# Performance work log

Hardware: AMD Instinct MI355X
Metric: run time of the kernel (lower is better)

Reference implementation:

```python
import jax, jax.numpy as jnp
import numpy as np

G = 8            # n_group
C = 256          # input_dim / channels
N_MEM = C // G   # 32
ALPHA = 0.4      # w_alpha
EPS = 1e-5
SLOPE = 0.01     # LeakyReLU negative slope


def _lrelu(x):
    return jnp.where(x >= 0, x, SLOPE * x)


def _mlp(x, ws, bs):
    # torch nn.Linear convention: y = x @ W.T + b; lrelu on all but last layer
    n = len(ws)
    for i in range(n):
        x = x @ ws[i].T + bs[i]
        if i < n - 1:
            x = _lrelu(x)
    return x


def _wct(c_A, s_B, mask, ct_ws, ct_bs, mu_ws, mu_bs):
    B, Cc, H, W = c_A.shape
    n_mem = Cc // G
    # style -> per-group coloring matrices  (Get.coloring, vectorized over groups)
    s_CT = _mlp(s_B.reshape(B * G, n_mem), ct_ws, ct_bs).reshape(B, G, n_mem, n_mem)
    D = jnp.sqrt(jnp.sum(s_CT ** 2, axis=2, keepdims=True))        # [B,G,1,n_mem]
    U = s_CT / D                                                    # column-normalized
    UDU = jnp.einsum('bgij,bgkj->bgik', s_CT, U)                    # [B,G,n_mem,n_mem]
    # torch.cat(U_arr, dim=0) is group-major: index g*B+b
    eigen_s = jnp.transpose(U, (1, 0, 2, 3)).reshape(G * B, n_mem, n_mem)
    X = jnp.tile(UDU.reshape(B, Cc, n_mem), (1, 1, G)) * mask       # [B,C,C]
    s_mu = _mlp(s_B, mu_ws, mu_bs)[:, :, None, None]                # [B,C,1,1]
    # per-group covariance of mean-centered content
    c_g = jnp.transpose(c_A, (1, 0, 2, 3)).reshape(G, n_mem, B * H * W)
    c_g = c_g - jnp.mean(c_g, axis=2, keepdims=True)
    cov_c = jnp.einsum('gin,gjn->gij', c_g, c_g) / (B * H * W - 1) \
        + EPS * jnp.eye(n_mem, dtype=c_A.dtype)
    # centered content, reinterpreted as [B, C, H*W] (matches torch view/permute)
    whitend = jnp.transpose(c_g.reshape(Cc, B, H * W), (1, 0, 2))
    colored = jnp.einsum('bcd,bdn->bcn', X, whitend).reshape(B, Cc, H, W)
    out = ALPHA * (colored + s_mu) + (1.0 - ALPHA) * c_A
    return out, cov_c, eigen_s


def setup_inputs():
    key = jax.random.key(0)
    ks = jax.random.split(key, 16)
    B, H, W = 4, 128, 128
    c_A = jax.random.normal(ks[0], (B, C, H, W), dtype=jnp.float32)
    s_B = jax.random.normal(ks[1], (B, C), dtype=jnp.float32)
    # block-diagonal group mask [1, C, C]
    m = np.zeros((C, C), dtype=np.float32)
    for g in range(G):
        m[g * N_MEM:(g + 1) * N_MEM, g * N_MEM:(g + 1) * N_MEM] = 1.0
    mask = jnp.asarray(m)[None]

    def lin(k, o, i):
        return jax.random.normal(k, (o, i), dtype=jnp.float32) * (1.0 / np.sqrt(i))

    inp = {'c_A': c_A, 's_B': s_B, 'mask': mask}
    dims_ct = [(256, 32), (256, 256), (256, 256), (256, 256), (1024, 256)]
    for j, (o, i) in enumerate(dims_ct):
        inp['ct_w%d' % j] = lin(ks[2 + j], o, i)
        inp['ct_b%d' % j] = jnp.zeros((o,), dtype=jnp.float32)
    dims_mu = [(256, 256), (256, 256), (256, 256)]
    for j, (o, i) in enumerate(dims_mu):
        inp['mu_w%d' % j] = lin(ks[8 + j], o, i)
        inp['mu_b%d' % j] = jnp.zeros((o,), dtype=jnp.float32)
    return inp


def reference(c_A, s_B, mask, ct_w0, ct_b0, ct_w1, ct_b1, ct_w2, ct_b2,
              ct_w3, ct_b3, ct_w4, ct_b4, mu_w0, mu_b0, mu_w1, mu_b1,
              mu_w2, mu_b2):
    ct_ws = (ct_w0, ct_w1, ct_w2, ct_w3, ct_w4)
    ct_bs = (ct_b0, ct_b1, ct_b2, ct_b3, ct_b4)
    mu_ws = (mu_w0, mu_w1, mu_w2)
    mu_bs = (mu_b0, mu_b1, mu_b2)
    return _wct(c_A, s_B, mask, ct_ws, ct_bs, mu_ws, mu_bs)
```

## Files before the change

### kernel.cpp

```cpp
#include <hip/hip_runtime.h>
#include <hip/hip_bf16.h>

typedef __bf16 bf16x8 __attribute__((ext_vector_type(8)));
typedef float  f32x16 __attribute__((ext_vector_type(16)));

#define ALPHA_W 0.4f
#define NTOT 65536.0f

#define OUT_MAIN 16777216
#define OUT_COV  (OUT_MAIN)
#define OUT_EIG  (OUT_MAIN + 8192)

#define WS_PSXY  0
#define WS_PSX   524288
#define WS_SMU   559104
#define WS_CT    560128

struct WP {
    const float* cw0; const float* cb0;
    const float* cw1; const float* cb1;
    const float* cw2; const float* cb2;
    const float* cw3; const float* cb3;
    const float* cw4; const float* cb4;
    const float* mw0; const float* mb0;
    const float* mw1; const float* mb1;
    const float* mw2; const float* mb2;
};

__device__ __forceinline__ float lrelu(float x) { return x >= 0.f ? x : 0.01f * x; }

__device__ __forceinline__ float dotg256(const float* __restrict__ w, const float* __restrict__ x) {
    float a0 = 0.f, a1 = 0.f, a2 = 0.f, a3 = 0.f;
    #pragma unroll
    for (int i = 0; i < 256; i += 16) {
        float4 w0 = *(const float4*)(w + i);
        float4 w1 = *(const float4*)(w + i + 4);
        float4 w2 = *(const float4*)(w + i + 8);
        float4 w3 = *(const float4*)(w + i + 12);
        float4 x0 = *(const float4*)(x + i);
        float4 x1 = *(const float4*)(x + i + 4);
        float4 x2 = *(const float4*)(x + i + 8);
        float4 x3 = *(const float4*)(x + i + 12);
        a0 = fmaf(w0.x, x0.x, a0); a0 = fmaf(w0.y, x0.y, a0);
        a0 = fmaf(w0.z, x0.z, a0); a0 = fmaf(w0.w, x0.w, a0);
        a1 = fmaf(w1.x, x1.x, a1); a1 = fmaf(w1.y, x1.y, a1);
        a1 = fmaf(w1.z, x1.z, a1); a1 = fmaf(w1.w, x1.w, a1);
        a2 = fmaf(w2.x, x2.x, a2); a2 = fmaf(w2.y, x2.y, a2);
        a2 = fmaf(w2.z, x2.z, a2); a2 = fmaf(w2.w, x2.w, a2);
        a3 = fmaf(w3.x, x3.x, a3); a3 = fmaf(w3.y, x3.y, a3);
        a3 = fmaf(w3.z, x3.z, a3); a3 = fmaf(w3.w, x3.w, a3);
    }
    return (a0 + a1) + (a2 + a3);
}

__global__ __launch_bounds__(256, 2) void fused_front(const float* __restrict__ cA,
                                                      const float* __restrict__ sB,
                                                      WP wp,
                                                      float* __restrict__ pSXY,
                                                      float* __restrict__ pSX,
                                                      float* __restrict__ CT,
                                                      float* __restrict__ SMU) {
    int bid = blockIdx.x;
    int tid = threadIdx.x;
    if (bid < 36) {
        __shared__ float xb_[256], hb_[256];
        int t = tid;
        if (bid < 32) {
            int r = bid;
            if (t < 32) xb_[t] = sB[r * 32 + t];
            __syncthreads();
            {
                const float* wr = wp.cw0 + t * 32;
                float a0 = 0.f, a1 = 0.f;
                #pragma unroll
                for (int i = 0; i < 32; i += 8) {
                    float4 u0 = *(const float4*)(wr + i);
                    float4 u1 = *(const float4*)(wr + i + 4);
                    float4 x0 = *(const float4*)(xb_ + i);
                    float4 x1 = *(const float4*)(xb_ + i + 4);
                    a0 = fmaf(u0.x, x0.x, a0); a0 = fmaf(u0.y, x0.y, a0);
                    a0 = fmaf(u0.z, x0.z, a0); a0 = fmaf(u0.w, x0.w, a0);
                    a1 = fmaf(u1.x, x1.x, a1); a1 = fmaf(u1.y, x1.y, a1);
                    a1 = fmaf(u1.z, x1.z, a1); a1 = fmaf(u1.w, x1.w, a1);
                }
                hb_[t] = lrelu(a0 + a1 + wp.cb0[t]);
            }
            __syncthreads();
            xb_[t] = lrelu(dotg256(wp.cw1 + (size_t)t * 256, hb_) + wp.cb1[t]);
            __syncthreads();
            hb_[t] = lrelu(dotg256(wp.cw2 + (size_t)t * 256, xb_) + wp.cb2[t]);
            __syncthreads();
            xb_[t] = lrelu(dotg256(wp.cw3 + (size_t)t * 256, hb_) + wp.cb3[t]);
            __syncthreads();
            #pragma unroll
            for (int c = 0; c < 4; c++) {
                int o = c * 256 + t;
                CT[(size_t)r * 1024 + o] = dotg256(wp.cw4 + (size_t)o * 256, xb_) + wp.cb4[o];
            }
        } else {
            int r = bid - 32;
            xb_[t] = sB[r * 256 + t];
            __syncthreads();
            hb_[t] = lrelu(dotg256(wp.mw0 + (size_t)t * 256, xb_) + wp.mb0[t]);
            __syncthreads();
            xb_[t] = lrelu(dotg256(wp.mw1 + (size_t)t * 256, hb_) + wp.mb1[t]);
            __syncthreads();
            SMU[r * 256 + t] = dotg256(wp.mw2 + (size_t)t * 256, xb_) + wp.mb2[t];
        }
        return;
    }
    int gbid = bid - 36;
    int g = gbid >> 6, slice = gbid & 63;
    int w = tid >> 6, l = tid & 63;
    int col = l & 31, kq = l >> 5;
    int nbase = slice * 1024 + w * 256;
    int b = nbase >> 14, hw0 = nbase & 16383;
    const float* base = cA + (((size_t)(b * 256 + g * 32 + col)) << 14) + hw0 + kq * 8;
    f32x16 acc;
    #pragma unroll
    for (int r = 0; r < 16; r++) acc[r] = 0.f;
    float s0 = 0.f, s1 = 0.f;
    #pragma unroll 8
    for (int it = 0; it < 16; ++it) {
        float4 f0 = *(const float4*)(base + it * 16);
        float4 f1 = *(const float4*)(base + it * 16 + 4);
        s0 += (f0.x + f0.y) + (f0.z + f0.w);
        s1 += (f1.x + f1.y) + (f1.z + f1.w);
        bf16x8 v;
        v[0] = (__bf16)f0.x; v[1] = (__bf16)f0.y; v[2] = (__bf16)f0.z; v[3] = (__bf16)f0.w;
        v[4] = (__bf16)f1.x; v[5] = (__bf16)f1.y; v[6] = (__bf16)f1.z; v[7] = (__bf16)f1.w;
        acc = __builtin_amdgcn_mfma_f32_32x32x16_bf16(v, v, acc, 0, 0, 0);
    }
    __shared__ float red[4][1024];
    __shared__ float sxr[4][64];
    sxr[w][l] = s0 + s1;
    #pragma unroll
    for (int r = 0; r < 16; r++) {
        int i = (r & 3) + 8 * (r >> 2) + 4 * kq;
        red[w][i * 32 + col] = acc[r];
    }
    __syncthreads();
    for (int e = tid; e < 1024; e += 256)
        pSXY[(size_t)gbid * 1024 + e] = red[0][e] + red[1][e] + red[2][e] + red[3][e];
    if (tid < 32) {
        float v = 0.f;
        #pragma unroll
        for (int ww = 0; ww < 4; ww++) v += sxr[ww][tid] + sxr[ww][tid + 32];
        pSX[gbid * 32 + tid] = v;
    }
}

__global__ __launch_bounds__(256) void color_fused(const float* __restrict__ cA,
                                                   const float* __restrict__ CT,
                                                   const float* __restrict__ SMU,
                                                   const float* __restrict__ pSX,
                                                   const float* __restrict__ pSXY,
                                                   float* __restrict__ out) {
    __shared__ float sct[32 * 33];
    __shared__ float sctd[32 * 33];
    __shared__ float Ml[1024];
    __shared__ float tl[32];
    __shared__ float sxg[32];
    __shared__ float dinv[32];
    __shared__ float xs[2][2048];
    int bid = blockIdx.x;
    int tid = threadIdx.x;

    if (bid >= 1024) {
        int g = bid - 1024;
        if (tid < 32) {
            float s = 0.f;
            #pragma unroll
            for (int sl = 0; sl < 64; sl++) s += pSX[(g * 64 + sl) * 32 + tid];
            sxg[tid] = s * (1.0f / NTOT);
        }
        __syncthreads();
        float* cov = out + OUT_COV + (size_t)g * 1024;
        for (int e = tid; e < 1024; e += 256) {
            float s = 0.f;
            #pragma unroll
            for (int sl = 0; sl < 64; sl++) s += pSXY[(size_t)(g * 64 + sl) * 1024 + e];
            int i = e >> 5, jj = e & 31;
            float vv = (s - NTOT * sxg[i] * sxg[jj]) * (1.0f / (NTOT - 1.0f));
            if (i == jj) vv += 1e-5f;
            cov[e] = vv;
        }
        return;
    }

    int bg = bid >> 5, chunk = bid & 31;
    int b = bg >> 3, g = bg & 7;

    for (int e = tid; e < 1024; e += 256) sct[(e >> 5) * 33 + (e & 31)] = CT[(size_t)bg * 1024 + e];
    if (tid < 32) {
        float s = 0.f;
        #pragma unroll
        for (int sl = 0; sl < 64; sl++) s += pSX[(g * 64 + sl) * 32 + tid];
        sxg[tid] = s * (1.0f / NTOT);
    }
    __syncthreads();
    if (tid < 32) {
        float s = 0.f;
        #pragma unroll
        for (int i = 0; i < 32; i++) { float v = sct[i * 33 + tid]; s = fmaf(v, v, s); }
        dinv[tid] = 1.0f / sqrtf(s);
    }
    __syncthreads();
    for (int e = tid; e < 1024; e += 256) {
        int i = e >> 5, j = e & 31;
        sctd[i * 33 + j] = sct[i * 33 + j] * dinv[j];
    }
    __syncthreads();
    if (chunk == 0) {
        float* eig = out + OUT_EIG + (size_t)(g * 4 + b) * 1024;
        for (int e = tid; e < 1024; e += 256) eig[e] = sctd[(e >> 5) * 33 + (e & 31)];
    }
    for (int e = tid; e < 1024; e += 256) {
        int i = e >> 5, k = e & 31;
        float s = 0.f;
        #pragma unroll
        for (int j = 0; j < 32; j++) s = fmaf(sct[i * 33 + j], sctd[k * 33 + j], s);
        Ml[e] = ALPHA_W * s + (i == k ? (1.0f - ALPHA_W) : 0.0f);
    }
    __syncthreads();
    if (tid < 32) {
        float s = 0.f;
        #pragma unroll
        for (int k = 0; k < 32; k++) s = fmaf(Ml[tid * 32 + k], sxg[k], s);
        tl[tid] = ALPHA_W * SMU[bg * 32 + tid] - s + (1.0f - ALPHA_W) * sxg[tid];
    }

    int n = tid & 63, ih = tid >> 6;
    size_t cbase = (((size_t)(b * 256 + g * 32)) << 14) + chunk * 512;
    int srow = tid >> 3, scol = (tid & 7) * 8;
    size_t obase = (((size_t)(b * 256 + g * 32 + ih * 8)) << 14) + chunk * 512 + n;
    for (int tile = 0; tile < 8; ++tile) {
        const float* src = cA + cbase + (size_t)srow * 16384 + tile * 64 + scol;
        float4 u0 = *(const float4*)src;
        float4 u1 = *(const float4*)(src + 4);
        float* xd = &xs[tile & 1][srow * 64 + scol];
        *(float4*)xd = u0;
        *(float4*)(xd + 4) = u1;
        __syncthreads();
        const float* xb = xs[tile & 1];
        float acc[8];
        #pragma unroll
        for (int i = 0; i < 8; i++) acc[i] = tl[ih * 8 + i];
        #pragma unroll
        for (int k = 0; k < 32; k++) {
            float xv = xb[k * 64 + n];
            #pragma unroll
            for (int i = 0; i < 8; i++) acc[i] = fmaf(Ml[(ih * 8 + i) * 32 + k], xv, acc[i]);
        }
        float* dst = out + obase + tile * 64;
        #pragma unroll
        for (int i = 0; i < 8; i++) dst[(size_t)i << 14] = acc[i];
    }
}

extern "C" void kernel_launch(void* const* d_in, const int* in_sizes, int n_in,
                              void* d_out, int out_size, void* d_ws, size_t ws_size,
                              hipStream_t stream) {
    (void)in_sizes; (void)n_in; (void)out_size; (void)ws_size;
    const float* cA = (const float*)d_in[0];
    const float* sB = (const float*)d_in[1];
    WP wp;
    wp.cw0 = (const float*)d_in[3];  wp.cb0 = (const float*)d_in[4];
    wp.cw1 = (const float*)d_in[5];  wp.cb1 = (const float*)d_in[6];
    wp.cw2 = (const float*)d_in[7];  wp.cb2 = (const float*)d_in[8];
    wp.cw3 = (const float*)d_in[9];  wp.cb3 = (const float*)d_in[10];
    wp.cw4 = (const float*)d_in[11]; wp.cb4 = (const float*)d_in[12];
    wp.mw0 = (const float*)d_in[13]; wp.mb0 = (const float*)d_in[14];
    wp.mw1 = (const float*)d_in[15]; wp.mb1 = (const float*)d_in[16];
    wp.mw2 = (const float*)d_in[17]; wp.mb2 = (const float*)d_in[18];
    float* W = (float*)d_ws;
    float* out = (float*)d_out;

    fused_front<<<548, 256, 0, stream>>>(cA, sB, wp, W + WS_PSXY, W + WS_PSX,
                                         W + WS_CT, W + WS_SMU);
    color_fused<<<1032, 256, 0, stream>>>(cA, W + WS_CT, W + WS_SMU,
                                          W + WS_PSX, W + WS_PSXY, out);
}
```

Measured before the change: 236.6 us.

## Batch style MLPs into two MFMA blocks with split-bf16 precision, prefetch color tiles

```diff
diff --git a/kernel.cpp b/kernel.cpp
--- a/kernel.cpp
+++ b/kernel.cpp
@@ -15,6 +15,8 @@
 #define WS_PSX   524288
 #define WS_SMU   559104
 #define WS_CT    560128
+
+#define XSTR 268
 
 struct WP {
     const float* cw0; const float* cb0;
@@ -29,87 +31,111 @@
 
 __device__ __forceinline__ float lrelu(float x) { return x >= 0.f ? x : 0.01f * x; }
 
-__device__ __forceinline__ float dotg256(const float* __restrict__ w, const float* __restrict__ x) {
-    float a0 = 0.f, a1 = 0.f, a2 = 0.f, a3 = 0.f;
-    #pragma unroll
-    for (int i = 0; i < 256; i += 16) {
-        float4 w0 = *(const float4*)(w + i);
-        float4 w1 = *(const float4*)(w + i + 4);
-        float4 w2 = *(const float4*)(w + i + 8);
-        float4 w3 = *(const float4*)(w + i + 12);
-        float4 x0 = *(const float4*)(x + i);
-        float4 x1 = *(const float4*)(x + i + 4);
-        float4 x2 = *(const float4*)(x + i + 8);
-        float4 x3 = *(const float4*)(x + i + 12);
-        a0 = fmaf(w0.x, x0.x, a0); a0 = fmaf(w0.y, x0.y, a0);
-        a0 = fmaf(w0.z, x0.z, a0); a0 = fmaf(w0.w, x0.w, a0);
-        a1 = fmaf(w1.x, x1.x, a1); a1 = fmaf(w1.y, x1.y, a1);
-        a1 = fmaf(w1.z, x1.z, a1); a1 = fmaf(w1.w, x1.w, a1);
-        a2 = fmaf(w2.x, x2.x, a2); a2 = fmaf(w2.y, x2.y, a2);
-        a2 = fmaf(w2.z, x2.z, a2); a2 = fmaf(w2.w, x2.w, a2);
-        a3 = fmaf(w3.x, x3.x, a3); a3 = fmaf(w3.y, x3.y, a3);
-        a3 = fmaf(w3.z, x3.z, a3); a3 = fmaf(w3.w, x3.w, a3);
-    }
-    return (a0 + a1) + (a2 + a3);
-}
-
-__global__ __launch_bounds__(256, 2) void fused_front(const float* __restrict__ cA,
-                                                      const float* __restrict__ sB,
-                                                      WP wp,
-                                                      float* __restrict__ pSXY,
-                                                      float* __restrict__ pSX,
-                                                      float* __restrict__ CT,
-                                                      float* __restrict__ SMU) {
+__device__ __forceinline__ void cvt8(const float4& a, const float4& b, bf16x8& h, bf16x8& l) {
+    float v[8] = {a.x, a.y, a.z, a.w, b.x, b.y, b.z, b.w};
+    #pragma unroll
+    for (int j = 0; j < 8; ++j) {
+        __bf16 hh = (__bf16)v[j];
+        h[j] = hh;
+        l[j] = (__bf16)(v[j] - (float)hh);
+    }
+}
+
+template<int NT, int K16, int ACT, int GLOB>
+__device__ __forceinline__ void layer_mfma(const float* __restrict__ Wg,
+                                           const float* __restrict__ Bs,
+                                           const float* __restrict__ Xin,
+                                           float* __restrict__ Xout,
+                                           float* __restrict__ Gout, int gld, int grows,
+                                           int obase0, int w, int ln, int hi, int in_dim) {
+    f32x16 acc[NT];
+    #pragma unroll
+    for (int t = 0; t < NT; ++t)
+        #pragma unroll
+        for (int r = 0; r < 16; ++r) acc[t][r] = 0.f;
+
+    #pragma unroll
+    for (int ks = 0; ks < K16; ++ks) {
+        int kof = ks * 16 + 8 * hi;
+        const float* ax = Xin + ln * XSTR + kof;
+        float4 a0 = *(const float4*)ax;
+        float4 a1 = *(const float4*)(ax + 4);
+        bf16x8 ah, al;
+        cvt8(a0, a1, ah, al);
+        #pragma unroll
+        for (int t = 0; t < NT; ++t) {
+            int ob = obase0 + (w * NT + t) * 32;
+            const float* bx = Wg + (size_t)(ob + ln) * in_dim + kof;
+            float4 b0 = *(const float4*)bx;
+            float4 b1 = *(const float4*)(bx + 4);
+            bf16x8 bh, bl;
+            cvt8(b0, b1, bh, bl);
+            acc[t] = __builtin_amdgcn_mfma_f32_32x32x16_bf16(ah, bh, acc[t], 0, 0, 0);
+            acc[t] = __builtin_amdgcn_mfma_f32_32x32x16_bf16(ah, bl, acc[t], 0, 0, 0);
+            acc[t] = __builtin_amdgcn_mfma_f32_32x32x16_bf16(al, bh, acc[t], 0, 0, 0);
+        }
+    }
+    #pragma unroll
+    for (int t = 0; t < NT; ++t) {
+        int ob = obase0 + (w * NT + t) * 32;
+        int o = ob + ln;
+        float bias = Bs[o];
+        #pragma unroll
+        for (int r = 0; r < 16; ++r) {
+            int row = (r & 3) + 8 * (r >> 2) + 4 * hi;
+            float v = acc[t][r] + bias;
+            if (ACT) v = lrelu(v);
+            if (GLOB) {
+                if (row < grows) Gout[(size_t)row * gld + o] = v;
+            } else {
+                Xout[row * XSTR + o] = v;
+            }
+        }
+    }
+}
+
+__global__ __launch_bounds__(256, 2) void front(const float* __restrict__ cA,
+                                                const float* __restrict__ sB,
+                                                WP wp,
+                                                float* __restrict__ pSXY,
+                                                float* __restrict__ pSX,
+                                                float* __restrict__ CT,
+                                                float* __restrict__ SMU) {
+    __shared__ float smem[2 * 32 * XSTR];
     int bid = blockIdx.x;
     int tid = threadIdx.x;
-    if (bid < 36) {
-        __shared__ float xb_[256], hb_[256];
-        int t = tid;
-        if (bid < 32) {
-            int r = bid;
-            if (t < 32) xb_[t] = sB[r * 32 + t];
-            __syncthreads();
-            {
-                const float* wr = wp.cw0 + t * 32;
-                float a0 = 0.f, a1 = 0.f;
-                #pragma unroll
-                for (int i = 0; i < 32; i += 8) {
-                    float4 u0 = *(const float4*)(wr + i);
-                    float4 u1 = *(const float4*)(wr + i + 4);
-                    float4 x0 = *(const float4*)(xb_ + i);
-                    float4 x1 = *(const float4*)(xb_ + i + 4);
-                    a0 = fmaf(u0.x, x0.x, a0); a0 = fmaf(u0.y, x0.y, a0);
-                    a0 = fmaf(u0.z, x0.z, a0); a0 = fmaf(u0.w, x0.w, a0);
-                    a1 = fmaf(u1.x, x1.x, a1); a1 = fmaf(u1.y, x1.y, a1);
-                    a1 = fmaf(u1.z, x1.z, a1); a1 = fmaf(u1.w, x1.w, a1);
-                }
-                hb_[t] = lrelu(a0 + a1 + wp.cb0[t]);
-            }
-            __syncthreads();
-            xb_[t] = lrelu(dotg256(wp.cw1 + (size_t)t * 256, hb_) + wp.cb1[t]);
-            __syncthreads();
-            hb_[t] = lrelu(dotg256(wp.cw2 + (size_t)t * 256, xb_) + wp.cb2[t]);
-            __syncthreads();
-            xb_[t] = lrelu(dotg256(wp.cw3 + (size_t)t * 256, hb_) + wp.cb3[t]);
-            __syncthreads();
-            #pragma unroll
-            for (int c = 0; c < 4; c++) {
-                int o = c * 256 + t;
-                CT[(size_t)r * 1024 + o] = dotg256(wp.cw4 + (size_t)o * 256, xb_) + wp.cb4[o];
-            }
+
+    if (bid < 2) {
+        float* XA = smem;
+        float* XB = smem + 32 * XSTR;
+        int ln = tid & 31, hi = (tid >> 5) & 1, w = tid >> 6;
+        if (bid == 0) {
+            for (int e = tid; e < 1024; e += 256) XA[(e >> 5) * XSTR + (e & 31)] = sB[e];
+            __syncthreads();
+            layer_mfma<2, 2, 1, 0>(wp.cw0, wp.cb0, XA, XB, nullptr, 0, 0, 0, w, ln, hi, 32);
+            __syncthreads();
+            layer_mfma<2, 16, 1, 0>(wp.cw1, wp.cb1, XB, XA, nullptr, 0, 0, 0, w, ln, hi, 256);
+            __syncthreads();
+            layer_mfma<2, 16, 1, 0>(wp.cw2, wp.cb2, XA, XB, nullptr, 0, 0, 0, w, ln, hi, 256);
+            __syncthreads();
+            layer_mfma<2, 16, 1, 0>(wp.cw3, wp.cb3, XB, XA, nullptr, 0, 0, 0, w, ln, hi, 256);
+            __syncthreads();
+            layer_mfma<4, 16, 0, 1>(wp.cw4, wp.cb4, XA, nullptr, CT, 1024, 32, 0, w, ln, hi, 256);
+            layer_mfma<4, 16, 0, 1>(wp.cw4, wp.cb4, XA, nullptr, CT, 1024, 32, 512, w, ln, hi, 256);
         } else {
-            int r = bid - 32;
-            xb_[t] = sB[r * 256 + t];
-            __syncthreads();
-            hb_[t] = lrelu(dotg256(wp.mw0 + (size_t)t * 256, xb_) + wp.mb0[t]);
-            __syncthreads();
-            xb_[t] = lrelu(dotg256(wp.mw1 + (size_t)t * 256, hb_) + wp.mb1[t]);
-            __syncthreads();
-            SMU[r * 256 + t] = dotg256(wp.mw2 + (size_t)t * 256, xb_) + wp.mb2[t];
+            for (int e = tid; e < 1024; e += 256) XA[(e >> 8) * XSTR + (e & 255)] = sB[e];
+            for (int e = tid; e < 28 * 256; e += 256) XA[(4 + (e >> 8)) * XSTR + (e & 255)] = 0.f;
+            __syncthreads();
+            layer_mfma<2, 16, 1, 0>(wp.mw0, wp.mb0, XA, XB, nullptr, 0, 0, 0, w, ln, hi, 256);
+            __syncthreads();
+            layer_mfma<2, 16, 1, 0>(wp.mw1, wp.mb1, XB, XA, nullptr, 0, 0, 0, w, ln, hi, 256);
+            __syncthreads();
+            layer_mfma<2, 16, 0, 1>(wp.mw2, wp.mb2, XA, nullptr, SMU, 256, 4, 0, w, ln, hi, 256);
         }
         return;
     }
-    int gbid = bid - 36;
+
+    int gbid = bid - 2;
     int g = gbid >> 6, slice = gbid & 63;
     int w = tid >> 6, l = tid & 63;
     int col = l & 31, kq = l >> 5;
@@ -131,21 +157,21 @@
         v[4] = (__bf16)f1.x; v[5] = (__bf16)f1.y; v[6] = (__bf16)f1.z; v[7] = (__bf16)f1.w;
         acc = __builtin_amdgcn_mfma_f32_32x32x16_bf16(v, v, acc, 0, 0, 0);
     }
-    __shared__ float red[4][1024];
-    __shared__ float sxr[4][64];
-    sxr[w][l] = s0 + s1;
+    float* red = smem;
+    float* sxr = smem + 4096;
+    sxr[w * 64 + l] = s0 + s1;
     #pragma unroll
     for (int r = 0; r < 16; r++) {
         int i = (r & 3) + 8 * (r >> 2) + 4 * kq;
-        red[w][i * 32 + col] = acc[r];
+        red[w * 1024 + i * 32 + col] = acc[r];
     }
     __syncthreads();
     for (int e = tid; e < 1024; e += 256)
-        pSXY[(size_t)gbid * 1024 + e] = red[0][e] + red[1][e] + red[2][e] + red[3][e];
+        pSXY[(size_t)gbid * 1024 + e] = red[e] + red[1024 + e] + red[2048 + e] + red[3072 + e];
     if (tid < 32) {
         float v = 0.f;
         #pragma unroll
-        for (int ww = 0; ww < 4; ww++) v += sxr[ww][tid] + sxr[ww][tid + 32];
+        for (int ww = 0; ww < 4; ww++) v += sxr[ww * 64 + tid] + sxr[ww * 64 + tid + 32];
         pSX[gbid * 32 + tid] = v;
     }
 }
@@ -234,13 +260,18 @@
     size_t cbase = (((size_t)(b * 256 + g * 32)) << 14) + chunk * 512;
     int srow = tid >> 3, scol = (tid & 7) * 8;
     size_t obase = (((size_t)(b * 256 + g * 32 + ih * 8)) << 14) + chunk * 512 + n;
+    const float* src0 = cA + cbase + (size_t)srow * 16384 + scol;
+    float4 u0 = *(const float4*)src0;
+    float4 u1 = *(const float4*)(src0 + 4);
     for (int tile = 0; tile < 8; ++tile) {
-        const float* src = cA + cbase + (size_t)srow * 16384 + tile * 64 + scol;
-        float4 u0 = *(const float4*)src;
-        float4 u1 = *(const float4*)(src + 4);
         float* xd = &xs[tile & 1][srow * 64 + scol];
         *(float4*)xd = u0;
         *(float4*)(xd + 4) = u1;
+        if (tile < 7) {
+            const float* src = cA + cbase + (size_t)srow * 16384 + (tile + 1) * 64 + scol;
+            u0 = *(const float4*)src;
+            u1 = *(const float4*)(src + 4);
+        }
         __syncthreads();
         const float* xb = xs[tile & 1];
         float acc[8];
@@ -276,8 +307,8 @@
     float* W = (float*)d_ws;
     float* out = (float*)d_out;
 
-    fused_front<<<548, 256, 0, stream>>>(cA, sB, wp, W + WS_PSXY, W + WS_PSX,
-                                         W + WS_CT, W + WS_SMU);
+    front<<<514, 256, 0, stream>>>(cA, sB, wp, W + WS_PSXY, W + WS_PSX,
+                                   W + WS_CT, W + WS_SMU);
     color_fused<<<1032, 256, 0, stream>>>(cA, W + WS_CT, W + WS_SMU,
                                           W + WS_PSX, W + WS_PSXY, out);
 }
```

Measured after the change: 280.8 us. 1.19x slower.

## Split style MLPs into per-layer multi-block stage kernels and prefetch color tiles

Applied to the files above, without the earlier changes.

```diff
diff --git a/kernel.cpp b/kernel.cpp
--- a/kernel.cpp
+++ b/kernel.cpp
@@ -13,6 +13,10 @@
 
 #define WS_PSXY  0
 #define WS_PSX   524288
+#define WS_XA    540672
+#define WS_XB    548864
+#define WS_MUA   557056
+#define WS_MUB   558080
 #define WS_SMU   559104
 #define WS_CT    560128
 
@@ -27,89 +31,60 @@
     const float* mw2; const float* mb2;
 };
 
+struct SJ { const float* X; const float* W; const float* B; float* Y; int ld; int act; };
+
 __device__ __forceinline__ float lrelu(float x) { return x >= 0.f ? x : 0.01f * x; }
 
-__device__ __forceinline__ float dotg256(const float* __restrict__ w, const float* __restrict__ x) {
+template<int ROWS, int IN, int KS, int NCB, int ACT>
+__device__ __forceinline__ void lin_block(const float* __restrict__ X,
+                                          const float* __restrict__ Wg,
+                                          const float* __restrict__ Bs,
+                                          float* __restrict__ Y, int ld,
+                                          int bidl, int tid) {
+    constexpr int SL = IN / KS;
+    constexpr int SF4 = SL / 4;
+    int s = tid % KS;
+    int r = (tid / KS) % ROWS;
+    int c = tid / (KS * ROWS);
+    int col = bidl * NCB + c;
+    const float4* wp = (const float4*)(Wg + (size_t)col * IN + s * SL);
+    const float4* xp = (const float4*)(X + r * IN + s * SL);
     float a0 = 0.f, a1 = 0.f, a2 = 0.f, a3 = 0.f;
     #pragma unroll
-    for (int i = 0; i < 256; i += 16) {
-        float4 w0 = *(const float4*)(w + i);
-        float4 w1 = *(const float4*)(w + i + 4);
-        float4 w2 = *(const float4*)(w + i + 8);
-        float4 w3 = *(const float4*)(w + i + 12);
-        float4 x0 = *(const float4*)(x + i);
-        float4 x1 = *(const float4*)(x + i + 4);
-        float4 x2 = *(const float4*)(x + i + 8);
-        float4 x3 = *(const float4*)(x + i + 12);
-        a0 = fmaf(w0.x, x0.x, a0); a0 = fmaf(w0.y, x0.y, a0);
-        a0 = fmaf(w0.z, x0.z, a0); a0 = fmaf(w0.w, x0.w, a0);
-        a1 = fmaf(w1.x, x1.x, a1); a1 = fmaf(w1.y, x1.y, a1);
-        a1 = fmaf(w1.z, x1.z, a1); a1 = fmaf(w1.w, x1.w, a1);
-        a2 = fmaf(w2.x, x2.x, a2); a2 = fmaf(w2.y, x2.y, a2);
-        a2 = fmaf(w2.z, x2.z, a2); a2 = fmaf(w2.w, x2.w, a2);
-        a3 = fmaf(w3.x, x3.x, a3); a3 = fmaf(w3.y, x3.y, a3);
-        a3 = fmaf(w3.z, x3.z, a3); a3 = fmaf(w3.w, x3.w, a3);
-    }
-    return (a0 + a1) + (a2 + a3);
-}
-
-__global__ __launch_bounds__(256, 2) void fused_front(const float* __restrict__ cA,
-                                                      const float* __restrict__ sB,
-                                                      WP wp,
-                                                      float* __restrict__ pSXY,
-                                                      float* __restrict__ pSX,
-                                                      float* __restrict__ CT,
-                                                      float* __restrict__ SMU) {
+    for (int i = 0; i < SF4; ++i) {
+        float4 wv = wp[i];
+        float4 xv = xp[i];
+        a0 = fmaf(wv.x, xv.x, a0); a1 = fmaf(wv.y, xv.y, a1);
+        a2 = fmaf(wv.z, xv.z, a2); a3 = fmaf(wv.w, xv.w, a3);
+    }
+    float v = (a0 + a1) + (a2 + a3);
+    #pragma unroll
+    for (int m = 1; m < KS; m <<= 1) v += __shfl_xor(v, m, 64);
+    if (s == 0) {
+        float o = v + Bs[col];
+        if (ACT) o = lrelu(o);
+        Y[(size_t)r * ld + col] = o;
+    }
+}
+
+__global__ __launch_bounds__(256, 2) void front(const float* __restrict__ cA,
+                                                const float* __restrict__ sB,
+                                                WP wp,
+                                                float* __restrict__ pSXY,
+                                                float* __restrict__ pSX,
+                                                float* __restrict__ XA,
+                                                float* __restrict__ MUA) {
     int bid = blockIdx.x;
     int tid = threadIdx.x;
-    if (bid < 36) {
-        __shared__ float xb_[256], hb_[256];
-        int t = tid;
+    if (bid < 64) {
         if (bid < 32) {
-            int r = bid;
-            if (t < 32) xb_[t] = sB[r * 32 + t];
-            __syncthreads();
-            {
-                const float* wr = wp.cw0 + t * 32;
-                float a0 = 0.f, a1 = 0.f;
-                #pragma unroll
-                for (int i = 0; i < 32; i += 8) {
-                    float4 u0 = *(const float4*)(wr + i);
-                    float4 u1 = *(const float4*)(wr + i + 4);
-                    float4 x0 = *(const float4*)(xb_ + i);
-                    float4 x1 = *(const float4*)(xb_ + i + 4);
-                    a0 = fmaf(u0.x, x0.x, a0); a0 = fmaf(u0.y, x0.y, a0);
-                    a0 = fmaf(u0.z, x0.z, a0); a0 = fmaf(u0.w, x0.w, a0);
-                    a1 = fmaf(u1.x, x1.x, a1); a1 = fmaf(u1.y, x1.y, a1);
-                    a1 = fmaf(u1.z, x1.z, a1); a1 = fmaf(u1.w, x1.w, a1);
-                }
-                hb_[t] = lrelu(a0 + a1 + wp.cb0[t]);
-            }
-            __syncthreads();
-            xb_[t] = lrelu(dotg256(wp.cw1 + (size_t)t * 256, hb_) + wp.cb1[t]);
-            __syncthreads();
-            hb_[t] = lrelu(dotg256(wp.cw2 + (size_t)t * 256, xb_) + wp.cb2[t]);
-            __syncthreads();
-            xb_[t] = lrelu(dotg256(wp.cw3 + (size_t)t * 256, hb_) + wp.cb3[t]);
-            __syncthreads();
-            #pragma unroll
-            for (int c = 0; c < 4; c++) {
-                int o = c * 256 + t;
-                CT[(size_t)r * 1024 + o] = dotg256(wp.cw4 + (size_t)o * 256, xb_) + wp.cb4[o];
-            }
+            lin_block<32, 32, 1, 8, 1>(sB, wp.cw0, wp.cb0, XA, 256, bid, tid);
         } else {
-            int r = bid - 32;
-            xb_[t] = sB[r * 256 + t];
-            __syncthreads();
-            hb_[t] = lrelu(dotg256(wp.mw0 + (size_t)t * 256, xb_) + wp.mb0[t]);
-            __syncthreads();
-            xb_[t] = lrelu(dotg256(wp.mw1 + (size_t)t * 256, hb_) + wp.mb1[t]);
-            __syncthreads();
-            SMU[r * 256 + t] = dotg256(wp.mw2 + (size_t)t * 256, xb_) + wp.mb2[t];
+            lin_block<4, 256, 8, 8, 1>(sB, wp.mw0, wp.mb0, MUA, 256, bid - 32, tid);
         }
         return;
     }
-    int gbid = bid - 36;
+    int gbid = bid - 64;
     int g = gbid >> 6, slice = gbid & 63;
     int w = tid >> 6, l = tid & 63;
     int col = l & 31, kq = l >> 5;
@@ -147,6 +122,18 @@
         #pragma unroll
         for (int ww = 0; ww < 4; ww++) v += sxr[ww][tid] + sxr[ww][tid + 32];
         pSX[gbid * 32 + tid] = v;
+    }
+}
+
+__global__ __launch_bounds__(256) void stage(SJ a, SJ m, int nbA) {
+    int bid = blockIdx.x, tid = threadIdx.x;
+    if (bid < nbA) {
+        if (a.act) lin_block<32, 256, 4, 2, 1>(a.X, a.W, a.B, a.Y, a.ld, bid, tid);
+        else       lin_block<32, 256, 4, 2, 0>(a.X, a.W, a.B, a.Y, a.ld, bid, tid);
+    } else {
+        int bl = bid - nbA;
+        if (m.act) lin_block<4, 256, 8, 8, 1>(m.X, m.W, m.B, m.Y, m.ld, bl, tid);
+        else       lin_block<4, 256, 8, 8, 0>(m.X, m.W, m.B, m.Y, m.ld, bl, tid);
     }
 }
 
@@ -234,13 +221,18 @@
     size_t cbase = (((size_t)(b * 256 + g * 32)) << 14) + chunk * 512;
     int srow = tid >> 3, scol = (tid & 7) * 8;
     size_t obase = (((size_t)(b * 256 + g * 32 + ih * 8)) << 14) + chunk * 512 + n;
+    const float* src0 = cA + cbase + (size_t)srow * 16384 + scol;
+    float4 u0 = *(const float4*)src0;
+    float4 u1 = *(const float4*)(src0 + 4);
     for (int tile = 0; tile < 8; ++tile) {
-        const float* src = cA + cbase + (size_t)srow * 16384 + tile * 64 + scol;
-        float4 u0 = *(const float4*)src;
-        float4 u1 = *(const float4*)(src + 4);
         float* xd = &xs[tile & 1][srow * 64 + scol];
         *(float4*)xd = u0;
         *(float4*)(xd + 4) = u1;
+        if (tile < 7) {
+            const float* src = cA + cbase + (size_t)srow * 16384 + (tile + 1) * 64 + scol;
+            u0 = *(const float4*)src;
+            u1 = *(const float4*)(src + 4);
+        }
         __syncthreads();
         const float* xb = xs[tile & 1];
         float acc[8];
@@ -276,8 +268,20 @@
     float* W = (float*)d_ws;
     float* out = (float*)d_out;
 
-    fused_front<<<548, 256, 0, stream>>>(cA, sB, wp, W + WS_PSXY, W + WS_PSX,
-                                         W + WS_CT, W + WS_SMU);
+    front<<<576, 256, 0, stream>>>(cA, sB, wp, W + WS_PSXY, W + WS_PSX,
+                                   W + WS_XA, W + WS_MUA);
+    SJ a, m;
+    a = {W + WS_XA, wp.cw1, wp.cb1, W + WS_XB, 256, 1};
+    m = {W + WS_MUA, wp.mw1, wp.mb1, W + WS_MUB, 256, 1};
+    stage<<<160, 256, 0, stream>>>(a, m, 128);
+    a = {W + WS_XB, wp.cw2, wp.cb2, W + WS_XA, 256, 1};
+    m = {W + WS_MUB, wp.mw2, wp.mb2, W + WS_SMU, 256, 0};
+    stage<<<160, 256, 0, stream>>>(a, m, 128);
+    a = {W + WS_XA, wp.cw3, wp.cb3, W + WS_XB, 256, 1};
+    stage<<<128, 256, 0, stream>>>(a, a, 128);
+    a = {W + WS_XB, wp.cw4, wp.cb4, W + WS_CT, 1024, 0};
+    stage<<<512, 256, 0, stream>>>(a, a, 512);
+
     color_fused<<<1032, 256, 0, stream>>>(cA, W + WS_CT, W + WS_SMU,
                                           W + WS_PSX, W + WS_PSXY, out);
 }
```

New measurement: 197.3 us, median of 2. 1.2x faster.
